# Kernel optimization log

Hardware: AMD Instinct MI355X
Metric: run time of the kernel (lower is better)

Reference implementation:

```python
import jax, jax.numpy as jnp
import numpy as np

B, N = 2048, 64
Q_SIZE, K_SIZE, HIDDEN, OUT_SIZE, N_HEAD = 512, 512, 128, 512, 8
LN_EPS = 1e-5


def setup_inputs() -> dict:
    key = jax.random.key(0)
    ks = jax.random.split(key, 9)
    s_q = 1.0 / np.sqrt(Q_SIZE)
    s_k = 1.0 / np.sqrt(K_SIZE)
    s_o = 1.0 / np.sqrt(N_HEAD * HIDDEN)
    return {
        "me": jax.random.normal(ks[0], (B, Q_SIZE), jnp.float32),
        "other": jax.random.normal(ks[1], (B, N, K_SIZE), jnp.float32),
        # stacked per-head projection weights (torch Linear applied as x @ W)
        "Wq": jax.random.normal(ks[2], (N_HEAD, Q_SIZE, HIDDEN), jnp.float32) * s_q,
        "bq": jnp.zeros((N_HEAD, HIDDEN), jnp.float32),
        "Wk": jax.random.normal(ks[3], (N_HEAD, K_SIZE, HIDDEN), jnp.float32) * s_k,
        "Wv": jax.random.normal(ks[4], (N_HEAD, K_SIZE, HIDDEN), jnp.float32) * s_k,
        "gamma": jnp.ones((N_HEAD * HIDDEN,), jnp.float32),
        "beta": jnp.zeros((N_HEAD * HIDDEN,), jnp.float32),
        "Wo": jax.random.normal(ks[5], (N_HEAD * HIDDEN, OUT_SIZE), jnp.float32) * s_o,
    }


def _mhat2(me, other, Wq, bq, Wk, Wv, gamma, beta, Wo):
    # per-head projections, batched over the head axis
    q = jnp.einsum("bq,hqd->bhd", me, Wq) + bq[None]          # [B,H,D]
    k = jnp.einsum("bnk,hkd->bhnd", other, Wk)                 # [B,H,N,D]
    v = jnp.einsum("bnk,hkd->bhnd", other, Wv)                 # [B,H,N,D]
    scale = 1.0 / jnp.sqrt(jnp.asarray(HIDDEN, me.dtype))
    a = jnp.einsum("bhd,bhnd->bhn", q, k) * scale              # [B,H,N]
    a = jax.nn.softmax(a, axis=-1)
    out = jnp.einsum("bhn,bhnd->bhd", a, v)                    # [B,H,D]
    c = out.reshape(out.shape[0], N_HEAD * HIDDEN)             # concat heads
    mu = jnp.mean(c, axis=-1, keepdims=True)
    var = jnp.mean(jnp.square(c - mu), axis=-1, keepdims=True)
    cn = (c - mu) * jax.lax.rsqrt(var + LN_EPS) * gamma + beta
    return jax.nn.relu(cn) @ Wo                                # [B,OUT]


def reference(me, other, Wq, bq, Wk, Wv, gamma, beta, Wo):
    return _mhat2(me, other, Wq, bq, Wk, Wv, gamma, beta, Wo)
```

## Files before the change

### kernel.cpp

```cpp
#include <hip/hip_runtime.h>
#include <math.h>

typedef __attribute__((ext_vector_type(4))) float f32x4;
typedef __attribute__((ext_vector_type(4))) unsigned int u32x4;
typedef __attribute__((ext_vector_type(8))) short s16x8;

#define SCALE_INV_SQRT_H 0.08838834764831845f

__device__ __forceinline__ unsigned short f2bf(float x){
  unsigned int u = __builtin_bit_cast(unsigned int, x);
  u += 0x7fffu + ((u >> 16) & 1u);
  return (unsigned short)(u >> 16);
}
__device__ __forceinline__ float bf2f(unsigned short s){
  unsigned int u = ((unsigned int)s) << 16;
  return __builtin_bit_cast(float, u);
}

__device__ __forceinline__ void bar_lds(){
  asm volatile("s_waitcnt lgkmcnt(0)" ::: "memory");
  __builtin_amdgcn_s_barrier();
}

__device__ __forceinline__ void gemm_core64(
    const unsigned short* __restrict__ Ag, int lda,
    const unsigned short* __restrict__ Bg, int ldb,
    int ksteps, unsigned short* As, unsigned short* Bs, f32x4 acc[2][4])
{
  const int t = threadIdx.x, lane = t & 63, w = t >> 6;
  const int m0 = (w >> 1) * 32, n0 = (w & 1) * 64;
  const int ra_ = t >> 2, ua = (t & 3) * 2;
  const int rb_ = t >> 1, ub = (t & 1) * 4;
  for (int kk = 0; kk < ksteps; kk++) {
    __syncthreads();
    const unsigned short* ga = Ag + (size_t)ra_ * lda + kk * 64;
    const unsigned short* gb = Bg + (size_t)rb_ * ldb + kk * 64;
#pragma unroll
    for (int q = 0; q < 2; q++) {
      u32x4 va = *(const u32x4*)(ga + (ua + q) * 8);
      ((u32x4*)(As + ra_ * 64))[(ua + q) ^ (ra_ & 7)] = va;
    }
#pragma unroll
    for (int q = 0; q < 4; q++) {
      u32x4 vb = *(const u32x4*)(gb + (ub + q) * 8);
      ((u32x4*)(Bs + rb_ * 64))[(ub + q) ^ (rb_ & 7)] = vb;
    }
    __syncthreads();
    s16x8 af[2][2], bfr[4][2];
#pragma unroll
    for (int ks = 0; ks < 2; ks++) {
      int sa = ks * 4 + (lane >> 4);
#pragma unroll
      for (int i = 0; i < 2; i++) {
        int ra = m0 + i * 16 + (lane & 15);
        af[i][ks] = *(const s16x8*)(As + ra * 64 + ((sa ^ (ra & 7)) << 3));
      }
#pragma unroll
      for (int j = 0; j < 4; j++) {
        int rb = n0 + j * 16 + (lane & 15);
        bfr[j][ks] = *(const s16x8*)(Bs + rb * 64 + ((sa ^ (rb & 7)) << 3));
      }
    }
#pragma unroll
    for (int ks = 0; ks < 2; ks++)
#pragma unroll
      for (int i = 0; i < 2; i++)
#pragma unroll
        for (int j = 0; j < 4; j++)
          acc[i][j] = __builtin_amdgcn_mfma_f32_16x16x32_bf16(af[i][ks], bfr[j][ks], acc[i][j], 0, 0, 0);
  }
}

__device__ __forceinline__ void gemm_core32(
    const unsigned short* __restrict__ Ag, int lda,
    const unsigned short* __restrict__ Bg, int ldb,
    int ksteps, unsigned short* As, unsigned short* Bs, f32x4 acc[2][2])
{
  const int t = threadIdx.x, lane = t & 63, w = t >> 6;
  const int m0 = (w >> 1) * 32, n0 = (w & 1) * 32;
  const int r_ = t >> 2, u_ = (t & 3) * 2;
  for (int kk = 0; kk < ksteps; kk++) {
    __syncthreads();
    const unsigned short* ga = Ag + (size_t)r_ * lda + kk * 64;
    const unsigned short* gb = Bg + (size_t)r_ * ldb + kk * 64;
#pragma unroll
    for (int q = 0; q < 2; q++) {
      u32x4 va = *(const u32x4*)(ga + (u_ + q) * 8);
      u32x4 vb = *(const u32x4*)(gb + (u_ + q) * 8);
      ((u32x4*)(As + r_ * 64))[(u_ + q) ^ (r_ & 7)] = va;
      ((u32x4*)(Bs + r_ * 64))[(u_ + q) ^ (r_ & 7)] = vb;
    }
    __syncthreads();
    s16x8 af[2][2], bfr[2][2];
#pragma unroll
    for (int ks = 0; ks < 2; ks++) {
      int sa = ks * 4 + (lane >> 4);
#pragma unroll
      for (int i = 0; i < 2; i++) {
        int ra = m0 + i * 16 + (lane & 15);
        af[i][ks] = *(const s16x8*)(As + ra * 64 + ((sa ^ (ra & 7)) << 3));
        int rb = n0 + i * 16 + (lane & 15);
        bfr[i][ks] = *(const s16x8*)(Bs + rb * 64 + ((sa ^ (rb & 7)) << 3));
      }
    }
#pragma unroll
    for (int ks = 0; ks < 2; ks++)
#pragma unroll
      for (int i = 0; i < 2; i++)
#pragma unroll
        for (int j = 0; j < 2; j++)
          acc[i][j] = __builtin_amdgcn_mfma_f32_16x16x32_bf16(af[i][ks], bfr[j][ks], acc[i][j], 0, 0, 0);
  }
}

__device__ __forceinline__ void transpose_tile(const float* __restrict__ src, int lda,
                                               unsigned short* __restrict__ dst, int ldb,
                                               int r0, int c0, unsigned short (*tile)[72])
{
  const int t = threadIdx.x;
  const int cc = (t & 15) * 4, rr = t >> 4;
#pragma unroll
  for (int j = 0; j < 4; j++) {
    int r = rr + j * 16;
    f32x4 v = *(const f32x4*)(src + (size_t)(r0 + r) * lda + c0 + cc);
#pragma unroll
    for (int q = 0; q < 4; q++) tile[r][cc + q] = f2bf(v[q]);
  }
  __syncthreads();
  const int c = t >> 2, rb = (t & 3) * 16;
  unsigned short o[16];
#pragma unroll
  for (int q = 0; q < 16; q++) o[q] = tile[rb + q][c];
  u32x4 p0, p1;
#pragma unroll
  for (int q = 0; q < 4; q++) {
    p0[q] = (unsigned)o[2 * q]     | ((unsigned)o[2 * q + 1] << 16);
    p1[q] = (unsigned)o[2 * q + 8] | ((unsigned)o[2 * q + 9] << 16);
  }
  unsigned short* dp = dst + (size_t)(c0 + c) * ldb + r0 + rb;
  *(u32x4*)dp = p0;
  *(u32x4*)(dp + 8) = p1;
}

__global__ __launch_bounds__(256) void k_conv(
  const float* __restrict__ me, const float* __restrict__ Wq, const float* __restrict__ Wk,
  const float* __restrict__ Wv, const float* __restrict__ Wo,
  unsigned short* __restrict__ me_b, unsigned short* __restrict__ wk_b,
  unsigned short* __restrict__ wqt, unsigned short* __restrict__ wvt,
  unsigned short* __restrict__ wot)
{
  __shared__ unsigned short tile[64][72];
  const int bid = blockIdx.x, t = threadIdx.x;
  if (bid < 512) {
    for (int v = bid * 256 + t; v < 393216; v += 512 * 256) {
      const float* sp; unsigned short* dp;
      if (v < 262144) { sp = me + 4 * (size_t)v; dp = me_b + 4 * (size_t)v; }
      else { int i = v - 262144; sp = Wk + 4 * (size_t)i; dp = wk_b + 4 * (size_t)i; }
      f32x4 x = *(const f32x4*)sp;
      unsigned long long pk = (unsigned long long)((unsigned)f2bf(x[0]) | ((unsigned)f2bf(x[1]) << 16))
                            | (((unsigned long long)((unsigned)f2bf(x[2]) | ((unsigned)f2bf(x[3]) << 16))) << 32);
      *(unsigned long long*)dp = pk;
    }
    return;
  }
  if (bid < 640) {
    int idx = bid - 512, h = idx >> 4, tl = idx & 15;
    transpose_tile(Wq + (size_t)h * 65536, 128, wqt + (size_t)h * 65536, 512,
                   (tl >> 1) * 64, (tl & 1) * 64, tile);
  } else if (bid < 768) {
    int idx = bid - 640, h = idx >> 4, tl = idx & 15;
    transpose_tile(Wv + (size_t)h * 65536, 128, wvt + (size_t)h * 65536, 512,
                   (tl >> 1) * 64, (tl & 1) * 64, tile);
  } else {
    int idx = bid - 768;
    transpose_tile(Wo, 512, wot, 1024, (idx >> 3) * 64, (idx & 7) * 64, tile);
  }
}

__global__ __launch_bounds__(256) void k_qu(const unsigned short* __restrict__ me_b,
                                            const unsigned short* __restrict__ wqt,
                                            const float* __restrict__ bq,
                                            const unsigned short* __restrict__ wk_b,
                                            unsigned short* __restrict__ T)
{
  __shared__ unsigned short St[2][128 * 64];
  __shared__ unsigned short Qs[64 * 128];
  int bid = blockIdx.x;
  int h = bid & 7, bm = bid >> 4, bnh = (bid >> 3) & 1;
  const int t = threadIdx.x, lane = t & 63, w = t >> 6;
  const int m0 = (w >> 1) * 32, n0 = (w & 1) * 64;
  f32x4 z = {0.f, 0.f, 0.f, 0.f};

  f32x4 qacc[2][4];
#pragma unroll
  for (int i = 0; i < 2; i++) for (int j = 0; j < 4; j++) qacc[i][j] = z;
  gemm_core64(me_b + (size_t)bm * 64 * 512, 512, wqt + (size_t)h * 65536, 512, 8, St[0], St[1], qacc);
#pragma unroll
  for (int i = 0; i < 2; i++)
#pragma unroll
    for (int j = 0; j < 4; j++) {
      int col = n0 + j * 16 + (lane & 15);
      float bqv = bq[h * 128 + col];
#pragma unroll
      for (int rg = 0; rg < 4; rg++) {
        int row = m0 + i * 16 + (lane >> 4) * 4 + rg;
        *(unsigned short*)((char*)Qs + row * 256 + ((((col >> 3) ^ (row & 15)) << 4)) + (col & 7) * 2)
            = f2bf(qacc[i][j][rg] + bqv);
      }
    }
  __syncthreads();

  const int rb_ = t >> 1, ub = (t & 1) * 4;
#pragma unroll
  for (int c = 0; c < 2; c++) {
    int bn = bnh * 2 + c;
    if (c) __syncthreads();
    {
      const unsigned short* gb = wk_b + (size_t)h * 65536 + (size_t)(bn * 128 + rb_) * 128;
#pragma unroll
      for (int kt = 0; kt < 2; kt++)
#pragma unroll
        for (int q = 0; q < 4; q++) {
          u32x4 vb = *(const u32x4*)(gb + kt * 64 + (ub + q) * 8);
          ((u32x4*)(St[kt] + rb_ * 64))[(ub + q) ^ (rb_ & 7)] = vb;
        }
    }
    __syncthreads();
    f32x4 acc[2][4];
#pragma unroll
    for (int i = 0; i < 2; i++) for (int j = 0; j < 4; j++) acc[i][j] = z;
#pragma unroll
    for (int kt = 0; kt < 2; kt++)
#pragma unroll
      for (int ks = 0; ks < 2; ks++) {
        s16x8 af[2], bf[4];
        int sa = ks * 4 + (lane >> 4);
        int gq = (kt * 2 + ks) * 4 + (lane >> 4);
#pragma unroll
        for (int i = 0; i < 2; i++) {
          int ra = m0 + i * 16 + (lane & 15);
          af[i] = *(const s16x8*)((char*)Qs + ra * 256 + ((gq ^ (ra & 15)) << 4));
        }
#pragma unroll
        for (int j = 0; j < 4; j++) {
          int rb = n0 + j * 16 + (lane & 15);
          bf[j] = *(const s16x8*)(St[kt] + rb * 64 + ((sa ^ (rb & 7)) << 3));
        }
#pragma unroll
        for (int i = 0; i < 2; i++)
#pragma unroll
          for (int j = 0; j < 4; j++)
            acc[i][j] = __builtin_amdgcn_mfma_f32_16x16x32_bf16(af[i], bf[j], acc[i][j], 0, 0, 0);
      }
#pragma unroll
    for (int i = 0; i < 2; i++)
#pragma unroll
      for (int j = 0; j < 4; j++) {
        int col = h * 512 + bn * 128 + n0 + j * 16 + (lane & 15);
#pragma unroll
        for (int rg = 0; rg < 4; rg++) {
          int row = bm * 64 + m0 + i * 16 + (lane >> 4) * 4 + rg;
          T[(size_t)row * 4096 + col] = f2bf(acc[i][j][rg] * SCALE_INV_SQRT_H);
        }
      }
  }
}

__global__ __launch_bounds__(256) void k_attn(const float* __restrict__ other,
                                              const unsigned short* __restrict__ T,
                                              unsigned short* __restrict__ wbuf)
{
  __shared__ unsigned short oth[64 * 512];
  __shared__ unsigned short t_lds[8 * 512];
  __shared__ float s_lds[8 * 66];
  __shared__ char a_raw[4 * 1056];
  const int b = blockIdx.x;
  const int t = threadIdx.x, l = t & 63, w = t >> 6;

  u32x4 tv[2];
  f32x4 ov[32];
  {
    const unsigned short* tp = T + (size_t)b * 4096 + (t >> 5) * 512 + (t & 31) * 16;
    tv[0] = *(const u32x4*)tp;
    tv[1] = *(const u32x4*)(tp + 8);
    const f32x4* gp = (const f32x4*)(other + (size_t)b * 32768 + (size_t)(t >> 2) * 512);
#pragma unroll
    for (int j = 0; j < 32; j++) ov[j] = gp[(t & 3) + j * 4];
  }
  {
    int row = t >> 5;
    int col0 = (t & 31) * 16;
#pragma unroll
    for (int i = 0; i < 2; i++) {
      int gr = (col0 >> 3) + i;
      *(u32x4*)((char*)t_lds + row * 1024 + ((gr ^ row) << 4)) = tv[i];
    }
  }
  {
    int n = t >> 2;
    int nx = n & 7;
#pragma unroll
    for (int j = 0; j < 32; j++) {
      int kf0 = (t & 3) * 4 + j * 16;
      unsigned int lo = (unsigned)f2bf(ov[j][0]) | ((unsigned)f2bf(ov[j][1]) << 16);
      unsigned int hi = (unsigned)f2bf(ov[j][2]) | ((unsigned)f2bf(ov[j][3]) << 16);
      unsigned long long pk = (unsigned long long)lo | ((unsigned long long)hi << 32);
      int g = kf0 >> 3;
      *(unsigned long long*)((char*)oth + n * 1024 + ((g ^ nx) << 4) + (kf0 & 7) * 2) = pk;
    }
  }
  bar_lds();

  {
    f32x4 sacc = {0.f, 0.f, 0.f, 0.f};
    int arow = l & 7;
    int bn = w * 16 + (l & 15);
    int bx = bn & 7;
#pragma unroll
    for (int kk = 0; kk < 16; kk++) {
      int gr = kk * 4 + (l >> 4);
      s16x8 af  = *(const s16x8*)((char*)t_lds + arow * 1024 + ((gr ^ arow) << 4));
      s16x8 bfv = *(const s16x8*)((char*)oth + bn * 1024 + ((gr ^ bx) << 4));
      sacc = __builtin_amdgcn_mfma_f32_16x16x32_bf16(af, bfv, sacc, 0, 0, 0);
    }
    int hbase = (l >> 4) * 4;
    if (hbase < 8) {
#pragma unroll
      for (int rg = 0; rg < 4; rg++) s_lds[(hbase + rg) * 66 + w * 16 + (l & 15)] = sacc[rg];
    }
  }
  bar_lds();

#pragma unroll
  for (int hh = 0; hh < 2; hh++) {
    int h = w * 2 + hh;
    float v = s_lds[h * 66 + l];
    float mx = v;
#pragma unroll
    for (int off = 32; off > 0; off >>= 1) mx = fmaxf(mx, __shfl_xor(mx, off));
    float p = __expf(v - mx);
    float sm = p;
#pragma unroll
    for (int off = 32; off > 0; off >>= 1) sm += __shfl_xor(sm, off);
    unsigned short ab = f2bf(p / sm);
#pragma unroll
    for (int rep = 0; rep < 4; rep++)
      *(unsigned short*)(a_raw + rep * 1056 + h * 128 + l * 2) = ab;
  }
  bar_lds();

  {
    int g = l >> 4;
    int klane = l & 15;
    int kf0 = w * 128 + klane * 8;
    const char* abase = a_raw + g * 1056;
    s16x8 a0[8], a1[8];
#pragma unroll
    for (int r = 0; r < 8; r++) {
      a0[r] = *(const s16x8*)(abase + (2 * g) * 128 + r * 16);
      a1[r] = *(const s16x8*)(abase + (2 * g + 1) * 128 + r * 16);
    }
    float acc0[8], acc1[8];
#pragma unroll
    for (int q = 0; q < 8; q++) { acc0[q] = 0.f; acc1[q] = 0.f; }
    const char* obase = (const char*)oth;
    int gsl = w * 16 + klane;
#pragma unroll
    for (int r = 0; r < 8; r++) {
#pragma unroll
      for (int jj = 0; jj < 8; jj++) {
        int n = r * 8 + jj;
        float av0 = bf2f((unsigned short)a0[r][jj]);
        float av1 = bf2f((unsigned short)a1[r][jj]);
        s16x8 o = *(const s16x8*)(obase + n * 1024 + ((gsl ^ (n & 7)) << 4));
#pragma unroll
        for (int q = 0; q < 8; q++) {
          float f = bf2f((unsigned short)o[q]);
          acc0[q] += av0 * f;
          acc1[q] += av1 * f;
        }
      }
    }
    int h0 = 2 * g, h1 = h0 + 1;
    u32x4 p0, p1;
#pragma unroll
    for (int q = 0; q < 4; q++) {
      p0[q] = (unsigned)f2bf(acc0[2 * q]) | ((unsigned)f2bf(acc0[2 * q + 1]) << 16);
      p1[q] = (unsigned)f2bf(acc1[2 * q]) | ((unsigned)f2bf(acc1[2 * q + 1]) << 16);
    }
    *(u32x4*)(wbuf + ((size_t)b * 8 + h0) * 512 + kf0) = p0;
    *(u32x4*)(wbuf + ((size_t)b * 8 + h1) * 512 + kf0) = p1;
  }
}

__global__ __launch_bounds__(256) void k_c(const unsigned short* __restrict__ wbuf,
                                           const unsigned short* __restrict__ wvt,
                                           unsigned short* __restrict__ cbuf)
{
  __shared__ unsigned short As[64 * 64], Bs[64 * 64];
  int bid = blockIdx.x;
  int h = bid & 7, rest = bid >> 3;
  int dn = rest & 1, bm = rest >> 1;
  f32x4 acc[2][2]; f32x4 z = {0.f, 0.f, 0.f, 0.f};
#pragma unroll
  for (int i = 0; i < 2; i++) for (int j = 0; j < 2; j++) acc[i][j] = z;
  gemm_core32(wbuf + ((size_t)bm * 64 * 8 + h) * 512, 4096,
              wvt + (size_t)h * 65536 + (size_t)dn * 64 * 512, 512, 8, As, Bs, acc);
  {
    const int t = threadIdx.x, lane = t & 63, w = t >> 6;
    const int m0 = (w >> 1) * 32, n0 = (w & 1) * 32;
    unsigned short* C = cbuf + (size_t)bm * 64 * 1024 + h * 128 + dn * 64;
#pragma unroll
    for (int i = 0; i < 2; i++)
#pragma unroll
      for (int j = 0; j < 2; j++) {
        int col = n0 + j * 16 + (lane & 15);
#pragma unroll
        for (int rg = 0; rg < 4; rg++) {
          int row = m0 + i * 16 + (lane >> 4) * 4 + rg;
          C[(size_t)row * 1024 + col] = f2bf(acc[i][j][rg]);
        }
      }
  }
}

__global__ __launch_bounds__(256) void k_out(const unsigned short* __restrict__ cbuf,
                                             const float* __restrict__ gamma,
                                             const float* __restrict__ beta,
                                             const unsigned short* __restrict__ wot,
                                             float* __restrict__ out)
{
  __shared__ unsigned short As[32 * 1024];
  __shared__ unsigned short Bs[64 * 64];
  int bid = blockIdx.x;
  int bm = bid >> 3, bn = bid & 7;
  const int t = threadIdx.x, lane = t & 63, w = t >> 6;
  {
    int r = t >> 3;
    const unsigned short* g = cbuf + (size_t)(bm * 32 + r) * 1024;
#pragma unroll
    for (int q = 0; q < 16; q++) {
      int u = (t & 7) + q * 8;
      u32x4 v = *(const u32x4*)(g + u * 8);
      ((u32x4*)(As + r * 1024))[u ^ (r & 7)] = v;
    }
  }
  float gv[16], bv[16];
#pragma unroll
  for (int si = 0; si < 2; si++)
#pragma unroll
    for (int j = 0; j < 8; j++) {
      int k = (lane + si * 64) * 8 + j;
      gv[si * 8 + j] = gamma[k];
      bv[si * 8 + j] = beta[k];
    }
  __syncthreads();
  for (int rr = 0; rr < 8; rr++) {
    int r = w * 8 + rr;
    float vals[16]; float sum = 0.f, sq = 0.f;
#pragma unroll
    for (int si = 0; si < 2; si++) {
      int s = lane + si * 64;
      s16x8 pv = *(const s16x8*)(As + r * 1024 + ((s ^ (r & 7)) << 3));
#pragma unroll
      for (int j = 0; j < 8; j++) { float f = bf2f((unsigned short)pv[j]); vals[si * 8 + j] = f; sum += f; sq += f * f; }
    }
#pragma unroll
    for (int off = 32; off > 0; off >>= 1) { sum += __shfl_xor(sum, off); sq += __shfl_xor(sq, off); }
    float mu = sum * (1.f / 1024.f);
    float var = sq * (1.f / 1024.f) - mu * mu;
    float rs = rsqrtf(var + 1e-5f);
#pragma unroll
    for (int si = 0; si < 2; si++) {
      int s = lane + si * 64;
      unsigned short o[8];
#pragma unroll
      for (int j = 0; j < 8; j++) {
        float f = (vals[si * 8 + j] - mu) * rs * gv[si * 8 + j] + bv[si * 8 + j];
        o[j] = f2bf(fmaxf(f, 0.f));
      }
      u32x4 pk;
      pk[0] = (unsigned)o[0] | ((unsigned)o[1] << 16);
      pk[1] = (unsigned)o[2] | ((unsigned)o[3] << 16);
      pk[2] = (unsigned)o[4] | ((unsigned)o[5] << 16);
      pk[3] = (unsigned)o[6] | ((unsigned)o[7] << 16);
      ((u32x4*)(As + r * 1024))[s ^ (r & 7)] = pk;
    }
  }
  const int wm = w >> 1, wn = w & 1;
  f32x4 acc[2]; f32x4 z = {0.f, 0.f, 0.f, 0.f};
#pragma unroll
  for (int j = 0; j < 2; j++) acc[j] = z;
  const unsigned short* Bg = wot + (size_t)bn * 64 * 1024;
  const int rB = t >> 2, uB = (t & 3) * 2;
  for (int kk = 0; kk < 16; kk++) {
    __syncthreads();
#pragma unroll
    for (int q = 0; q < 2; q++) {
      u32x4 vb = *(const u32x4*)(Bg + (size_t)rB * 1024 + kk * 64 + (uB + q) * 8);
      ((u32x4*)(Bs + rB * 64))[(uB + q) ^ (rB & 7)] = vb;
    }
    __syncthreads();
#pragma unroll
    for (int ks = 0; ks < 2; ks++) {
      int ra = wm * 16 + (lane & 15);
      int sa = kk * 8 + ks * 4 + (lane >> 4);
      s16x8 af = *(const s16x8*)(As + ra * 1024 + ((sa ^ (ra & 7)) << 3));
      int sb = ks * 4 + (lane >> 4);
#pragma unroll
      for (int j = 0; j < 2; j++) {
        int rb = wn * 32 + j * 16 + (lane & 15);
        s16x8 bfv = *(const s16x8*)(Bs + rb * 64 + ((sb ^ (rb & 7)) << 3));
        acc[j] = __builtin_amdgcn_mfma_f32_16x16x32_bf16(af, bfv, acc[j], 0, 0, 0);
      }
    }
  }
#pragma unroll
  for (int j = 0; j < 2; j++) {
    int col = bn * 64 + wn * 32 + j * 16 + (lane & 15);
#pragma unroll
    for (int rg = 0; rg < 4; rg++) {
      int row = bm * 32 + wm * 16 + (lane >> 4) * 4 + rg;
      out[(size_t)row * 512 + col] = acc[j][rg];
    }
  }
}

extern "C" void kernel_launch(void* const* d_in, const int* in_sizes, int n_in,
                              void* d_out, int out_size, void* d_ws, size_t ws_size,
                              hipStream_t stream)
{
  (void)in_sizes; (void)n_in; (void)out_size;
  const float* me    = (const float*)d_in[0];
  const float* other = (const float*)d_in[1];
  const float* Wq    = (const float*)d_in[2];
  const float* bq    = (const float*)d_in[3];
  const float* Wk    = (const float*)d_in[4];
  const float* Wv    = (const float*)d_in[5];
  const float* gamma = (const float*)d_in[6];
  const float* beta  = (const float*)d_in[7];
  const float* Wo    = (const float*)d_in[8];
  float* out = (float*)d_out;
  char* ws = (char*)d_ws;

  unsigned short* me_b = (unsigned short*)(ws + 0);
  unsigned short* wk_b = (unsigned short*)(ws + 2097152);
  unsigned short* wqt  = (unsigned short*)(ws + 3145728);
  unsigned short* wvt  = (unsigned short*)(ws + 4194304);
  unsigned short* wot  = (unsigned short*)(ws + 5242880);
  unsigned short* T_b  = (unsigned short*)(ws + 10485760);
  unsigned short* w_b  = (unsigned short*)(ws + 27262976);
  unsigned short* c_b  = (unsigned short*)(ws + 44040192);
  if (ws_size < 48234496) return;

  k_conv<<<dim3(896),  dim3(256), 0, stream>>>(me, Wq, Wk, Wv, Wo, me_b, wk_b, wqt, wvt, wot);
  k_qu  <<<dim3(512),  dim3(256), 0, stream>>>(me_b, wqt, bq, wk_b, T_b);
  k_attn<<<dim3(2048), dim3(256), 0, stream>>>(other, T_b, w_b);
  k_c   <<<dim3(512),  dim3(256), 0, stream>>>(w_b, wvt, c_b);
  k_out <<<dim3(512),  dim3(256), 0, stream>>>(c_b, gamma, beta, wot, out);
}
```

Baseline: 110.0 us.

## Register-prefetch next K-tile global loads to overlap with MFMA compute

Each GEMM main loop (gemm_core64, gemm_core32, the Wk stage in k_qu, and the Wo output GEMM) now loads the next K-tile from global memory into registers right after the LDS barrier. The MFMA work on the current tile then overlaps that latency, and the registers are stored to LDS at the start of the next iteration. In k_qu the first Wk tile is also fetched before the Q epilogue so that load overlaps the bias add and Q store. This hides global load latency that used to sit between barriers, at the cost of extra VGPRs that may reduce occupancy.

```diff
diff --git a/kernel.cpp b/kernel.cpp
--- a/kernel.cpp
+++ b/kernel.cpp
@@ -31,21 +31,32 @@
   const int m0 = (w >> 1) * 32, n0 = (w & 1) * 64;
   const int ra_ = t >> 2, ua = (t & 3) * 2;
   const int rb_ = t >> 1, ub = (t & 1) * 4;
+  u32x4 va[2], vb[4];
+  {
+    const unsigned short* ga = Ag + (size_t)ra_ * lda;
+    const unsigned short* gb = Bg + (size_t)rb_ * ldb;
+#pragma unroll
+    for (int q = 0; q < 2; q++) va[q] = *(const u32x4*)(ga + (ua + q) * 8);
+#pragma unroll
+    for (int q = 0; q < 4; q++) vb[q] = *(const u32x4*)(gb + (ub + q) * 8);
+  }
   for (int kk = 0; kk < ksteps; kk++) {
     __syncthreads();
-    const unsigned short* ga = Ag + (size_t)ra_ * lda + kk * 64;
-    const unsigned short* gb = Bg + (size_t)rb_ * ldb + kk * 64;
-#pragma unroll
-    for (int q = 0; q < 2; q++) {
-      u32x4 va = *(const u32x4*)(ga + (ua + q) * 8);
-      ((u32x4*)(As + ra_ * 64))[(ua + q) ^ (ra_ & 7)] = va;
-    }
-#pragma unroll
-    for (int q = 0; q < 4; q++) {
-      u32x4 vb = *(const u32x4*)(gb + (ub + q) * 8);
-      ((u32x4*)(Bs + rb_ * 64))[(ub + q) ^ (rb_ & 7)] = vb;
-    }
+#pragma unroll
+    for (int q = 0; q < 2; q++)
+      ((u32x4*)(As + ra_ * 64))[(ua + q) ^ (ra_ & 7)] = va[q];
+#pragma unroll
+    for (int q = 0; q < 4; q++)
+      ((u32x4*)(Bs + rb_ * 64))[(ub + q) ^ (rb_ & 7)] = vb[q];
     __syncthreads();
+    if (kk + 1 < ksteps) {
+      const unsigned short* ga = Ag + (size_t)ra_ * lda + (kk + 1) * 64;
+      const unsigned short* gb = Bg + (size_t)rb_ * ldb + (kk + 1) * 64;
+#pragma unroll
+      for (int q = 0; q < 2; q++) va[q] = *(const u32x4*)(ga + (ua + q) * 8);
+#pragma unroll
+      for (int q = 0; q < 4; q++) vb[q] = *(const u32x4*)(gb + (ub + q) * 8);
+    }
     s16x8 af[2][2], bfr[4][2];
 #pragma unroll
     for (int ks = 0; ks < 2; ks++) {
@@ -79,18 +90,33 @@
   const int t = threadIdx.x, lane = t & 63, w = t >> 6;
   const int m0 = (w >> 1) * 32, n0 = (w & 1) * 32;
   const int r_ = t >> 2, u_ = (t & 3) * 2;
+  u32x4 va[2], vb[2];
+  {
+    const unsigned short* ga = Ag + (size_t)r_ * lda;
+    const unsigned short* gb = Bg + (size_t)r_ * ldb;
+#pragma unroll
+    for (int q = 0; q < 2; q++) {
+      va[q] = *(const u32x4*)(ga + (u_ + q) * 8);
+      vb[q] = *(const u32x4*)(gb + (u_ + q) * 8);
+    }
+  }
   for (int kk = 0; kk < ksteps; kk++) {
     __syncthreads();
-    const unsigned short* ga = Ag + (size_t)r_ * lda + kk * 64;
-    const unsigned short* gb = Bg + (size_t)r_ * ldb + kk * 64;
 #pragma unroll
     for (int q = 0; q < 2; q++) {
-      u32x4 va = *(const u32x4*)(ga + (u_ + q) * 8);
-      u32x4 vb = *(const u32x4*)(gb + (u_ + q) * 8);
-      ((u32x4*)(As + r_ * 64))[(u_ + q) ^ (r_ & 7)] = va;
-      ((u32x4*)(Bs + r_ * 64))[(u_ + q) ^ (r_ & 7)] = vb;
+      ((u32x4*)(As + r_ * 64))[(u_ + q) ^ (r_ & 7)] = va[q];
+      ((u32x4*)(Bs + r_ * 64))[(u_ + q) ^ (r_ & 7)] = vb[q];
     }
     __syncthreads();
+    if (kk + 1 < ksteps) {
+      const unsigned short* ga = Ag + (size_t)r_ * lda + (kk + 1) * 64;
+      const unsigned short* gb = Bg + (size_t)r_ * ldb + (kk + 1) * 64;
+#pragma unroll
+      for (int q = 0; q < 2; q++) {
+        va[q] = *(const u32x4*)(ga + (u_ + q) * 8);
+        vb[q] = *(const u32x4*)(gb + (u_ + q) * 8);
+      }
+    }
     s16x8 af[2][2], bfr[2][2];
 #pragma unroll
     for (int ks = 0; ks < 2; ks++) {
@@ -195,6 +221,18 @@
 #pragma unroll
   for (int i = 0; i < 2; i++) for (int j = 0; j < 4; j++) qacc[i][j] = z;
   gemm_core64(me_b + (size_t)bm * 64 * 512, 512, wqt + (size_t)h * 65536, 512, 8, St[0], St[1], qacc);
+
+  const int rb_ = t >> 1, ub = (t & 1) * 4;
+  u32x4 wv[2][4];
+  {
+    const unsigned short* gb = wk_b + (size_t)h * 65536 + (size_t)((bnh * 2) * 128 + rb_) * 128;
+#pragma unroll
+    for (int kt = 0; kt < 2; kt++)
+#pragma unroll
+      for (int q = 0; q < 4; q++)
+        wv[kt][q] = *(const u32x4*)(gb + kt * 64 + (ub + q) * 8);
+  }
+
 #pragma unroll
   for (int i = 0; i < 2; i++)
 #pragma unroll
@@ -210,22 +248,24 @@
     }
   __syncthreads();
 
-  const int rb_ = t >> 1, ub = (t & 1) * 4;
 #pragma unroll
   for (int c = 0; c < 2; c++) {
     int bn = bnh * 2 + c;
     if (c) __syncthreads();
-    {
-      const unsigned short* gb = wk_b + (size_t)h * 65536 + (size_t)(bn * 128 + rb_) * 128;
+#pragma unroll
+    for (int kt = 0; kt < 2; kt++)
+#pragma unroll
+      for (int q = 0; q < 4; q++)
+        ((u32x4*)(St[kt] + rb_ * 64))[(ub + q) ^ (rb_ & 7)] = wv[kt][q];
+    __syncthreads();
+    if (c == 0) {
+      const unsigned short* gb = wk_b + (size_t)h * 65536 + (size_t)((bnh * 2 + 1) * 128 + rb_) * 128;
 #pragma unroll
       for (int kt = 0; kt < 2; kt++)
 #pragma unroll
-        for (int q = 0; q < 4; q++) {
-          u32x4 vb = *(const u32x4*)(gb + kt * 64 + (ub + q) * 8);
-          ((u32x4*)(St[kt] + rb_ * 64))[(ub + q) ^ (rb_ & 7)] = vb;
-        }
-    }
-    __syncthreads();
+        for (int q = 0; q < 4; q++)
+          wv[kt][q] = *(const u32x4*)(gb + kt * 64 + (ub + q) * 8);
+    }
     f32x4 acc[2][4];
 #pragma unroll
     for (int i = 0; i < 2; i++) for (int j = 0; j < 4; j++) acc[i][j] = z;
@@ -493,14 +533,21 @@
   for (int j = 0; j < 2; j++) acc[j] = z;
   const unsigned short* Bg = wot + (size_t)bn * 64 * 1024;
   const int rB = t >> 2, uB = (t & 3) * 2;
+  u32x4 pv[2];
+#pragma unroll
+  for (int q = 0; q < 2; q++)
+    pv[q] = *(const u32x4*)(Bg + (size_t)rB * 1024 + (uB + q) * 8);
   for (int kk = 0; kk < 16; kk++) {
     __syncthreads();
 #pragma unroll
-    for (int q = 0; q < 2; q++) {
-      u32x4 vb = *(const u32x4*)(Bg + (size_t)rB * 1024 + kk * 64 + (uB + q) * 8);
-      ((u32x4*)(Bs + rB * 64))[(uB + q) ^ (rB & 7)] = vb;
-    }
+    for (int q = 0; q < 2; q++)
+      ((u32x4*)(Bs + rB * 64))[(uB + q) ^ (rB & 7)] = pv[q];
     __syncthreads();
+    if (kk < 15) {
+#pragma unroll
+      for (int q = 0; q < 2; q++)
+        pv[q] = *(const u32x4*)(Bg + (size_t)rB * 1024 + (kk + 1) * 64 + (uB + q) * 8);
+    }
 #pragma unroll
     for (int ks = 0; ks < 2; ks++) {
       int ra = wm * 16 + (lane & 15);
```

Result: faster. 104.3 us (median of 2 runs) (-5.2%).
